# Kernel optimization log

Hardware: AMD Instinct MI355X
Metric: run time of the kernel (lower is better)

The kernel has to match this reference:

```python
import jax, jax.numpy as jnp
import numpy as np

D_MODEL = 1024
N_Q = 16
N_KV = 4
HEAD = 64
T = 4096
B = 1


def setup_inputs() -> dict:
    key = jax.random.key(0)
    ks = jax.random.split(key, 5)
    q_dim = N_Q * HEAD
    kv_dim = N_KV * HEAD
    s = 0.02
    return {
        "x": jax.random.normal(ks[0], (B, T, D_MODEL), dtype=jnp.float32),
        "W_q": jax.random.normal(ks[1], (D_MODEL, q_dim), dtype=jnp.float32) * s,
        "W_k": jax.random.normal(ks[2], (D_MODEL, kv_dim), dtype=jnp.float32) * s,
        "W_v": jax.random.normal(ks[3], (D_MODEL, kv_dim), dtype=jnp.float32) * s,
        "W_o": jax.random.normal(ks[4], (q_dim, D_MODEL), dtype=jnp.float32) * s,
    }


def reference(x, W_q, W_k, W_v, W_o):
    Bsz, Tlen, _ = x.shape
    n_q_per_kv = N_Q // N_KV
    scale = jnp.asarray(np.sqrt(HEAD), x.dtype)
    # projections, split heads: (B, T, H*D) -> (B, H, T, D)
    q = (x @ W_q).reshape(Bsz, Tlen, N_Q, HEAD).transpose(0, 2, 1, 3)
    k = (x @ W_k).reshape(Bsz, Tlen, N_KV, HEAD).transpose(0, 2, 1, 3)
    v = (x @ W_v).reshape(Bsz, Tlen, N_KV, HEAD).transpose(0, 2, 1, 3)
    # GQA: duplicate KV heads to match query heads (repeat_interleave on head dim)
    k = jnp.repeat(k, n_q_per_kv, axis=1)
    v = jnp.repeat(v, n_q_per_kv, axis=1)
    attn = jnp.einsum("bhqd,bhkd->bhqk", q, k) / scale  # (B, H, T, T)
    causal = jnp.tril(jnp.ones((Tlen, Tlen), dtype=bool))
    attn = jnp.where(causal[None, None], attn, -jnp.inf)
    attn = jax.nn.softmax(attn, axis=-1)
    out = jnp.einsum("bhqk,bhkd->bhqd", attn, v)  # (B, H, T, D)
    out = out.transpose(0, 2, 1, 3).reshape(Bsz, Tlen, N_Q * HEAD)
    return out @ W_o
```

## Files before the change

kernel.cpp:

```cpp
#include <hip/hip_runtime.h>

typedef __bf16 bf16;
typedef __bf16 bf16x4 __attribute__((ext_vector_type(4)));
typedef __bf16 bf16x8 __attribute__((ext_vector_type(8)));
typedef float  f32x4  __attribute__((ext_vector_type(4)));

#define DEV __device__ __forceinline__

#if __has_builtin(__builtin_amdgcn_exp2f)
#define EXP2(x) __builtin_amdgcn_exp2f(x)
#else
#define EXP2(x) exp2f(x)
#endif

DEV void gload16(const void* g, void* l) {
  __builtin_amdgcn_global_load_lds((const __attribute__((address_space(1))) void*)g,
                                   (__attribute__((address_space(3))) void*)l, 16, 0, 0);
}

DEV f32x4 mfma16(bf16x8 a, bf16x8 b, f32x4 c) {
  return __builtin_amdgcn_mfma_f32_16x16x32_bf16(a, b, c, 0, 0, 0);
}

#define QSCALE 0.18033688011112042f

__global__ __launch_bounds__(256) void prep_kernel(const float* __restrict__ x,
                                                   const float* __restrict__ Wq,
                                                   const float* __restrict__ Wk,
                                                   const float* __restrict__ Wv,
                                                   const float* __restrict__ Wo,
                                                   bf16* __restrict__ xb,
                                                   bf16* __restrict__ wqkvt,
                                                   bf16* __restrict__ wot) {
  __shared__ float tile[32][33];
  int bid = blockIdx.x;
  if (bid < 4096) {
    int i = bid * 256 + threadIdx.x;
    f32x4 v = ((const f32x4*)x)[i];
    bf16x4 o = {(bf16)v.x, (bf16)v.y, (bf16)v.z, (bf16)v.w};
    ((bf16x4*)xb)[i] = o;
    return;
  }
  const float* src; int ld, nb; bf16* dst; int idx;
  if (bid < 5632) {
    idx = bid - 4096; dst = wqkvt;
    int n0 = (idx >> 5) * 32;
    if (n0 < 1024)      { src = Wq; ld = 1024; nb = 0; }
    else if (n0 < 1280) { src = Wk; ld = 256;  nb = 1024; }
    else                { src = Wv; ld = 256;  nb = 1280; }
  } else {
    idx = bid - 5632; dst = wot; src = Wo; ld = 1024; nb = 0;
  }
  int k0 = (idx & 31) * 32, n0 = (idx >> 5) * 32;
  int tx = threadIdx.x & 31, ty = threadIdx.x >> 5;
#pragma unroll
  for (int i = 0; i < 4; i++) {
    int r = ty + 8 * i;
    tile[r][tx] = src[(size_t)(k0 + r) * ld + (n0 - nb + tx)];
  }
  __syncthreads();
#pragma unroll
  for (int i = 0; i < 4; i++) {
    int r = ty + 8 * i;
    dst[(size_t)(n0 + r) * 1024 + k0 + tx] = (bf16)tile[tx][r];
  }
}

template <int MODE>
__global__ __launch_bounds__(256) void gemm_kernel(const bf16* __restrict__ A,
                                                   const bf16* __restrict__ B,
                                                   float* __restrict__ Cf,
                                                   bf16* __restrict__ qkbuf,
                                                   bf16* __restrict__ vtbuf, int N) {
  constexpr int K = 1024;
  __shared__ bf16 Al[2][64 * 64];
  __shared__ bf16 Bl[2][128 * 64];
  int tid = threadIdx.x;
  int w = tid >> 6, lane = tid & 63;
  int g = lane >> 4, r15 = lane & 15;
  int wr = w >> 1, wc = w & 1;
  int m0 = blockIdx.y * 64, n0 = blockIdx.x * 128;

  int sl = lane & 7;
  int srw = lane >> 3;
  const bf16* Abase = A + (size_t)m0 * K;
  const bf16* Bbase = B + (size_t)n0 * K;

#define GSTAGE(kk_, b_) do { \
    _Pragma("unroll") \
    for (int i = 0; i < 2; i++) { \
      int ra = 16 * w + 8 * i + srw; \
      gload16(Abase + (size_t)ra * K + (kk_) + 8 * (sl ^ (ra & 7)), \
              (char*)Al[b_] + (16 * w + 8 * i) * 128); \
    } \
    _Pragma("unroll") \
    for (int i = 0; i < 4; i++) { \
      int rb = 32 * w + 8 * i + srw; \
      gload16(Bbase + (size_t)rb * K + (kk_) + 8 * (sl ^ (rb & 7)), \
              (char*)Bl[b_] + (32 * w + 8 * i) * 128); \
    } \
  } while (0)

  GSTAGE(0, 0);
  __syncthreads();

  f32x4 acc[2][4] = {};
  for (int kk = 0; kk < K; kk += 64) {
    int cur = (kk >> 6) & 1;
    if (kk + 64 < K) GSTAGE(kk + 64, cur ^ 1);
    bf16x8 af[2][2], bb[4][2];
#pragma unroll
    for (int mi = 0; mi < 2; mi++) {
      int m = 32 * wr + 16 * mi + r15;
#pragma unroll
      for (int ks = 0; ks < 2; ks++)
        af[mi][ks] = *(const bf16x8*)((const char*)Al[cur] + m * 128 + 16 * ((4 * ks + g) ^ (m & 7)));
    }
#pragma unroll
    for (int ni = 0; ni < 4; ni++) {
      int n = 64 * wc + 16 * ni + r15;
#pragma unroll
      for (int ks = 0; ks < 2; ks++)
        bb[ni][ks] = *(const bf16x8*)((const char*)Bl[cur] + n * 128 + 16 * ((4 * ks + g) ^ (n & 7)));
    }
    __builtin_amdgcn_s_setprio(1);
#pragma unroll
    for (int ks = 0; ks < 2; ks++)
#pragma unroll
      for (int mi = 0; mi < 2; mi++)
#pragma unroll
        for (int ni = 0; ni < 4; ni++)
          acc[mi][ni] = mfma16(af[mi][ks], bb[ni][ks], acc[mi][ni]);
    __builtin_amdgcn_s_setprio(0);
    __syncthreads();
  }

  if (MODE == 0) {
#pragma unroll
    for (int mi = 0; mi < 2; mi++) {
      int mg = m0 + 32 * wr + 16 * mi + 4 * g;
#pragma unroll
      for (int ni = 0; ni < 4; ni++) {
        int ng = n0 + 64 * wc + 16 * ni + r15;
#pragma unroll
        for (int r = 0; r < 4; r++)
          Cf[(size_t)(mg + r) * N + ng] = acc[mi][ni][r];
      }
    }
  } else {
    if (n0 < 1280) {
      float qs = (n0 < 1024) ? QSCALE : 1.0f;
#pragma unroll
      for (int mi = 0; mi < 2; mi++) {
        int tg = m0 + 32 * wr + 16 * mi + 4 * g;
#pragma unroll
        for (int ni = 0; ni < 4; ni++) {
          int ng = n0 + 64 * wc + 16 * ni + r15;
#pragma unroll
          for (int r = 0; r < 4; r++)
            qkbuf[(size_t)(tg + r) * 1280 + ng] = (bf16)(acc[mi][ni][r] * qs);
        }
      }
    } else {
#pragma unroll
      for (int mi = 0; mi < 2; mi++) {
        int tg = m0 + 32 * wr + 16 * mi + 4 * g;
#pragma unroll
        for (int ni = 0; ni < 4; ni++) {
          int vcol = n0 + 64 * wc + 16 * ni + r15 - 1280;
          bf16x4 pk = {(bf16)acc[mi][ni][0], (bf16)acc[mi][ni][1],
                       (bf16)acc[mi][ni][2], (bf16)acc[mi][ni][3]};
          *(bf16x4*)(vtbuf + (size_t)vcol * 4096 + tg) = pk;
        }
      }
    }
  }
#undef GSTAGE
}

__global__ __launch_bounds__(256) void attn_kernel(const bf16* __restrict__ qk,
                                                   const bf16* __restrict__ vt,
                                                   bf16* __restrict__ out) {
  __shared__ bf16 Kt[2][64 * 64];
  __shared__ bf16 Vt[2][64 * 64];
  __shared__ bf16 Pl[4][16][72];
  int tid = threadIdx.x, w = tid >> 6, lane = tid & 63;
  int g = lane >> 4, r15 = lane & 15;
  int j = blockIdx.x;
  int h = j & 15, tI = 63 - (j >> 4);
  int kh = h >> 2;
  int na = tI + 1;
  int qw = 64 * tI + 16 * w;

  bf16x8 bq[2];
#pragma unroll
  for (int ks = 0; ks < 2; ks++)
    bq[ks] = *(const bf16x8*)(qk + (size_t)(qw + r15) * 1280 + h * 64 + 32 * ks + 8 * g);

  float l_run = 0.f;
  f32x4 oacc[4] = {};

  int sw8 = 8 * ((lane & 7) ^ (lane >> 3));
  const bf16* kbase = qk + 1024 + (size_t)kh * 64 + (size_t)(16 * w + (lane >> 3)) * 1280 + sw8;
  const bf16* vbase = vt + ((size_t)(kh * 64 + 16 * w + (lane >> 3))) * 4096 + sw8;

#define STAGE(t0_, b_) do { \
    char* kd = (char*)Kt[b_] + w * 2048; \
    char* vd = (char*)Vt[b_] + w * 2048; \
    gload16(kbase + (size_t)(t0_) * 1280, kd); \
    gload16(kbase + (size_t)(t0_) * 1280 + (size_t)8 * 1280, kd + 1024); \
    gload16(vbase + (t0_), vd); \
    gload16(vbase + (t0_) + 8 * 4096, vd + 1024); \
  } while (0)

  STAGE(0, 0);
  __syncthreads();

  for (int it = 0; it < na; ++it) {
    int cur = it & 1;
    int t0 = 64 * it;
    if (it + 1 < na) STAGE(64 * (it + 1), cur ^ 1);
    bool need_mask = (it == na - 1);
    const char* Kc = (const char*)Kt[cur];
    const char* Vc = (const char*)Vt[cur];

    f32x4 s[4];
    __builtin_amdgcn_s_setprio(1);
#pragma unroll
    for (int mi = 0; mi < 4; mi++) {
      int kv = 16 * mi + r15;
      bf16x8 k0f = *(const bf16x8*)(Kc + kv * 128 + 16 * (g ^ (kv & 7)));
      bf16x8 k1f = *(const bf16x8*)(Kc + kv * 128 + 16 * ((4 + g) ^ (kv & 7)));
      f32x4 z = {};
      z = mfma16(k0f, bq[0], z);
      z = mfma16(k1f, bq[1], z);
      s[mi] = z;
    }
    __builtin_amdgcn_s_setprio(0);

    int qg = qw + r15;
    float psum = 0.f;
    bf16 pb[16];
#pragma unroll
    for (int mi = 0; mi < 4; mi++)
#pragma unroll
      for (int r = 0; r < 4; r++) {
        float v = s[mi][r];
        if (need_mask) {
          int kvg = t0 + 16 * mi + 4 * g + r;
          v = (kvg > qg) ? -1e30f : v;
        }
        float pp = EXP2(v);
        psum += pp;
        pb[4 * mi + r] = (bf16)pp;
      }
    l_run += psum;

#pragma unroll
    for (int mi = 0; mi < 4; mi++) {
      bf16x4 pk = {pb[4 * mi], pb[4 * mi + 1], pb[4 * mi + 2], pb[4 * mi + 3]};
      *(bf16x4*)((char*)&Pl[w][r15][0] + mi * 32 + g * 8) = pk;
    }
    bf16x8 ap0 = *(const bf16x8*)((const char*)&Pl[w][r15][0] + 16 * g);
    bf16x8 ap1 = *(const bf16x8*)((const char*)&Pl[w][r15][0] + 64 + 16 * g);
    __builtin_amdgcn_s_setprio(1);
#pragma unroll
    for (int ni = 0; ni < 4; ni++) {
      int d = 16 * ni + r15;
      bf16x8 bv0 = *(const bf16x8*)(Vc + d * 128 + 16 * (g ^ (d & 7)));
      bf16x8 bv1 = *(const bf16x8*)(Vc + d * 128 + 16 * ((4 + g) ^ (d & 7)));
      oacc[ni] = mfma16(ap0, bv0, oacc[ni]);
      oacc[ni] = mfma16(ap1, bv1, oacc[ni]);
    }
    __builtin_amdgcn_s_setprio(0);
    __syncthreads();
  }
#undef STAGE

  float lsum = l_run;
  lsum += __shfl_xor(lsum, 16);
  lsum += __shfl_xor(lsum, 32);
  float linv = 1.0f / lsum;
  float li[4];
#pragma unroll
  for (int r = 0; r < 4; r++) li[r] = __shfl(linv, 4 * g + r);
#pragma unroll
  for (int ni = 0; ni < 4; ni++)
#pragma unroll
    for (int r = 0; r < 4; r++)
      out[(size_t)(qw + 4 * g + r) * 1024 + h * 64 + 16 * ni + r15] =
          (bf16)(oacc[ni][r] * li[r]);
}

extern "C" void kernel_launch(void* const* d_in, const int* in_sizes, int n_in,
                              void* d_out, int out_size, void* d_ws, size_t ws_size,
                              hipStream_t stream) {
  const float* x  = (const float*)d_in[0];
  const float* Wq = (const float*)d_in[1];
  const float* Wk = (const float*)d_in[2];
  const float* Wv = (const float*)d_in[3];
  const float* Wo = (const float*)d_in[4];
  float* out = (float*)d_out;
  char* ws = (char*)d_ws;
  bf16* xb    = (bf16*)(ws);
  bf16* wqkvt = (bf16*)(ws + 8388608);
  bf16* wot   = (bf16*)(ws + 11534336);
  bf16* qkbuf = (bf16*)(ws + 13631488);
  bf16* vtb   = (bf16*)(ws + 24117248);

  prep_kernel<<<6656, 256, 0, stream>>>(x, Wq, Wk, Wv, Wo, xb, wqkvt, wot);
  gemm_kernel<1><<<dim3(12, 64), 256, 0, stream>>>(xb, wqkvt, nullptr, qkbuf, vtb, 1536);
  attn_kernel<<<dim3(1024), 256, 0, stream>>>(qkbuf, vtb, xb);
  gemm_kernel<0><<<dim3(8, 64), 256, 0, stream>>>(xb, wot, out, nullptr, nullptr, 1024);
}
```

Measured before the change: 173.4 us.

## Load V fragments directly from global, remap GEMM blocks for XCD locality

The attention kernel drops the LDS staging buffer for V and instead has each lane load its MFMA B-operand fragments straight from global memory into registers at the start of each KV tile. This removes half the async LDS traffic and frees shared memory, and a launch-bounds occupancy hint of 4 is added. The GEMM kernels switch to a 1D grid with a block-index remap that groups consecutive tiles onto the same XCD (bid&7 chunking) to improve L2 reuse. The cost is that V loads are no longer prefetched a tile ahead, so global latency may be exposed and register pressure rises.

Measured after the change: 267.4 us. 1.54x slower.

```diff
diff --git a/kernel.cpp b/kernel.cpp
--- a/kernel.cpp
+++ b/kernel.cpp
@@ -66,7 +66,7 @@
   }
 }
 
-template <int MODE>
+template <int MODE, int NBX, int CHUNK>
 __global__ __launch_bounds__(256) void gemm_kernel(const bf16* __restrict__ A,
                                                    const bf16* __restrict__ B,
                                                    float* __restrict__ Cf,
@@ -79,7 +79,10 @@
   int w = tid >> 6, lane = tid & 63;
   int g = lane >> 4, r15 = lane & 15;
   int wr = w >> 1, wc = w & 1;
-  int m0 = blockIdx.y * 64, n0 = blockIdx.x * 128;
+  int bid = blockIdx.x;
+  int f = (bid & 7) * CHUNK + (bid >> 3);
+  int bx = f % NBX, by = f / NBX;
+  int m0 = by * 64, n0 = bx * 128;
 
   int sl = lane & 7;
   int srw = lane >> 3;
@@ -178,11 +181,10 @@
 #undef GSTAGE
 }
 
-__global__ __launch_bounds__(256) void attn_kernel(const bf16* __restrict__ qk,
-                                                   const bf16* __restrict__ vt,
-                                                   bf16* __restrict__ out) {
+__global__ __launch_bounds__(256, 4) void attn_kernel(const bf16* __restrict__ qk,
+                                                      const bf16* __restrict__ vt,
+                                                      bf16* __restrict__ out) {
   __shared__ bf16 Kt[2][64 * 64];
-  __shared__ bf16 Vt[2][64 * 64];
   __shared__ bf16 Pl[4][16][72];
   int tid = threadIdx.x, w = tid >> 6, lane = tid & 63;
   int g = lane >> 4, r15 = lane & 15;
@@ -202,15 +204,12 @@
 
   int sw8 = 8 * ((lane & 7) ^ (lane >> 3));
   const bf16* kbase = qk + 1024 + (size_t)kh * 64 + (size_t)(16 * w + (lane >> 3)) * 1280 + sw8;
-  const bf16* vbase = vt + ((size_t)(kh * 64 + 16 * w + (lane >> 3))) * 4096 + sw8;
+  const bf16* vbase = vt + (size_t)(kh * 64 + r15) * 4096 + 8 * g;
 
 #define STAGE(t0_, b_) do { \
     char* kd = (char*)Kt[b_] + w * 2048; \
-    char* vd = (char*)Vt[b_] + w * 2048; \
     gload16(kbase + (size_t)(t0_) * 1280, kd); \
     gload16(kbase + (size_t)(t0_) * 1280 + (size_t)8 * 1280, kd + 1024); \
-    gload16(vbase + (t0_), vd); \
-    gload16(vbase + (t0_) + 8 * 4096, vd + 1024); \
   } while (0)
 
   STAGE(0, 0);
@@ -219,10 +218,17 @@
   for (int it = 0; it < na; ++it) {
     int cur = it & 1;
     int t0 = 64 * it;
+
+    bf16x8 bv[4][2];
+#pragma unroll
+    for (int ni = 0; ni < 4; ni++)
+#pragma unroll
+      for (int ks = 0; ks < 2; ks++)
+        bv[ni][ks] = *(const bf16x8*)(vbase + (size_t)ni * 65536 + 32 * ks + t0);
+
     if (it + 1 < na) STAGE(64 * (it + 1), cur ^ 1);
     bool need_mask = (it == na - 1);
     const char* Kc = (const char*)Kt[cur];
-    const char* Vc = (const char*)Vt[cur];
 
     f32x4 s[4];
     __builtin_amdgcn_s_setprio(1);
@@ -266,11 +272,8 @@
     __builtin_amdgcn_s_setprio(1);
 #pragma unroll
     for (int ni = 0; ni < 4; ni++) {
-      int d = 16 * ni + r15;
-      bf16x8 bv0 = *(const bf16x8*)(Vc + d * 128 + 16 * (g ^ (d & 7)));
-      bf16x8 bv1 = *(const bf16x8*)(Vc + d * 128 + 16 * ((4 + g) ^ (d & 7)));
-      oacc[ni] = mfma16(ap0, bv0, oacc[ni]);
-      oacc[ni] = mfma16(ap1, bv1, oacc[ni]);
+      oacc[ni] = mfma16(ap0, bv[ni][0], oacc[ni]);
+      oacc[ni] = mfma16(ap1, bv[ni][1], oacc[ni]);
     }
     __builtin_amdgcn_s_setprio(0);
     __syncthreads();
@@ -309,7 +312,7 @@
   bf16* vtb   = (bf16*)(ws + 24117248);
 
   prep_kernel<<<6656, 256, 0, stream>>>(x, Wq, Wk, Wv, Wo, xb, wqkvt, wot);
-  gemm_kernel<1><<<dim3(12, 64), 256, 0, stream>>>(xb, wqkvt, nullptr, qkbuf, vtb, 1536);
-  attn_kernel<<<dim3(1024), 256, 0, stream>>>(qkbuf, vtb, xb);
-  gemm_kernel<0><<<dim3(8, 64), 256, 0, stream>>>(xb, wot, out, nullptr, nullptr, 1024);
-}
+  gemm_kernel<1, 12, 96><<<768, 256, 0, stream>>>(xb, wqkvt, nullptr, qkbuf, vtb, 1536);
+  attn_kernel<<<1024, 256, 0, stream>>>(qkbuf, vtb, xb);
+  gemm_kernel<0, 8, 64><<<512, 256, 0, stream>>>(xb, wot, out, nullptr, nullptr, 1024);
+}
```
